# Performance work log

Hardware: AMD Instinct MI355X
Metric: run time of the kernel (lower is better)

Reference implementation:

```python
import jax, jax.numpy as jnp
import numpy as np

B, S, D, H, R, N, KR = 2, 2048, 1024, 16, 256, 8, 128
DH = D // H
EPS = 1e-5


def setup_inputs() -> dict:
    key = jax.random.key(0)
    ks = jax.random.split(key, 20)
    sm = lambda k, n: jax.nn.softmax(jax.random.normal(k, (B, S, n), jnp.float32), axis=-1)
    return {
        "x": jax.random.normal(ks[0], (B, S, D), jnp.float32),
        "fqk_w_Q": sm(ks[1], N),
        "fqk_w_K": sm(ks[2], N),
        "fv_w": sm(ks[3], N),
        "rqk_w_Q": sm(ks[4], N),
        "rqk_w_K": sm(ks[5], N),
        "rv_w": sm(ks[6], N),
        "feature_know_w": sm(ks[7], N),
        "restore_know_w": sm(ks[8], N),
        "f_qk": jax.random.normal(ks[9], (N, D, R), jnp.float32) * 0.02,
        "f_v": jax.random.normal(ks[10], (N, D, R), jnp.float32) * 0.02,
        "r_qk": jax.random.normal(ks[11], (N, R, D), jnp.float32) * 0.02,
        "r_v": jax.random.normal(ks[12], (N, R, D), jnp.float32) * 0.02,
        "f_know": jax.random.normal(ks[13], (N, D, KR), jnp.float32) * 0.02,
        "r_know": jax.random.normal(ks[14], (N, KR, D), jnp.float32) * 0.02,
        "W_O": jax.random.normal(ks[15], (D, D), jnp.float32) * 0.02,
        "ln1_g": jnp.ones((D,), jnp.float32),
        "ln1_b": jnp.zeros((D,), jnp.float32),
        "ln2_g": jnp.ones((D,), jnp.float32),
        "ln2_b": jnp.zeros((D,), jnp.float32),
    }


def _layernorm(x, g, b):
    m = jnp.mean(x, axis=-1, keepdims=True)
    v = jnp.mean(jnp.square(x - m), axis=-1, keepdims=True)
    return (x - m) * jax.lax.rsqrt(v + EPS) * g + b


def _feature(x, neurons, w):
    # fused form of einsum('bsd,ndr->bsnr') + einsum('bsnr,bsn->bsr')
    return jnp.einsum('bsd,bsn,ndr->bsr', x, w, neurons)


def _restore(h, neurons, w):
    # fused form of einsum('bsr,nrd->bsnd') + einsum('bsnd,bsn->bsd')
    return jnp.einsum('bsr,bsn,nrd->bsd', h, w, neurons)


def _causal_sdpa(q, k, v):
    # q,k,v: [B,H,S,DH]
    scores = jnp.einsum('bhqd,bhkd->bhqk', q, k) / jnp.sqrt(jnp.float32(DH))
    mask = jnp.tril(jnp.ones((S, S), bool))
    scores = jnp.where(mask, scores, jnp.finfo(scores.dtype).min)
    p = jax.nn.softmax(scores, axis=-1)
    return jnp.einsum('bhqk,bhkd->bhqd', p, v)


def _block(x, fqk_w_Q, fqk_w_K, fv_w, rqk_w_Q, rqk_w_K, rv_w,
           feature_know_w, restore_know_w, f_qk, f_v, r_qk, r_v,
           f_know, r_know, W_O, ln1_g, ln1_b, ln2_g, ln2_b):
    nx = _layernorm(x, ln1_g, ln1_b)
    h_q = _feature(nx, f_qk, fqk_w_Q)
    h_k = _feature(nx, f_qk, fqk_w_K)
    h_v = _feature(nx, f_v, fv_w)
    Q = _restore(h_q, r_qk, rqk_w_Q)
    K = _restore(h_k, r_qk, rqk_w_K)
    V = _restore(h_v, r_v, rv_w)
    to_heads = lambda t: t.reshape(B, S, H, DH).transpose(0, 2, 1, 3)
    attn = _causal_sdpa(to_heads(Q), to_heads(K), to_heads(V))
    attn = attn.transpose(0, 2, 1, 3).reshape(B, S, D)
    attn_out = attn @ W_O.T  # nn.Linear(d_model,d_model,bias=False)
    x = x + attn_out
    nx2 = _layernorm(x, ln2_g, ln2_b)
    h = _feature(nx2, f_know, feature_know_w)
    know_out = _restore(h, r_know, restore_know_w)
    return x + know_out


def reference(x, fqk_w_Q, fqk_w_K, fv_w, rqk_w_Q, rqk_w_K, rv_w,
              feature_know_w, restore_know_w, f_qk, f_v, r_qk, r_v,
              f_know, r_know, W_O, ln1_g, ln1_b, ln2_g, ln2_b):
    return _block(x, fqk_w_Q, fqk_w_K, fv_w, rqk_w_Q, rqk_w_K, rv_w,
                  feature_know_w, restore_know_w, f_qk, f_v, r_qk, r_v,
                  f_know, r_know, W_O, ln1_g, ln1_b, ln2_g, ln2_b)
```

## Files before the change

### kernel.cpp

```cpp
#include <hip/hip_runtime.h>
#include <hip/hip_bf16.h>


typedef __bf16 bf16_t;
typedef __bf16 bf16x8 __attribute__((ext_vector_type(8)));
typedef float f32x4 __attribute__((ext_vector_type(4)));

#define B_DIM 2
#define S_LEN 2048
#define D_DIM 1024
#define H_NUM 16
#define DH 64
#define N_NEU 8
#define R_DIM 256
#define KR_DIM 128
#define ROWS (B_DIM * S_LEN)

static __device__ __forceinline__ void gl_lds16(const void* g, void* l)
{
    __builtin_amdgcn_global_load_lds(
        (__attribute__((address_space(1))) void*)(g),
        (__attribute__((address_space(3))) void*)(l), 16, 0, 0);
}

__global__ __launch_bounds__(256)
void tcast_kernel(const float* __restrict__ in, bf16_t* __restrict__ out, int I, int J)
{
    __shared__ float t[32][33];
    const int bJ = blockIdx.x * 32, bI = blockIdx.y * 32;
    const size_t boff = (size_t)blockIdx.z * I * J;
    const int tx = threadIdx.x, ty = threadIdx.y;
#pragma unroll
    for (int i = 0; i < 4; i++)
        t[ty * 4 + i][tx] = in[boff + (size_t)(bI + ty * 4 + i) * J + bJ + tx];
    __syncthreads();
#pragma unroll
    for (int i = 0; i < 4; i++)
        out[boff + (size_t)(bJ + ty * 4 + i) * I + bI + tx] = (bf16_t)t[tx][ty * 4 + i];
}

__global__ __launch_bounds__(256)
void tbf_kernel(const bf16_t* __restrict__ in, bf16_t* __restrict__ out, int I, int J)
{
    __shared__ bf16_t t[32][33];
    const int bJ = blockIdx.x * 32, bI = blockIdx.y * 32;
    const size_t boff = (size_t)blockIdx.z * I * J;
    const int tx = threadIdx.x, ty = threadIdx.y;
#pragma unroll
    for (int i = 0; i < 4; i++)
        t[ty * 4 + i][tx] = in[boff + (size_t)(bI + ty * 4 + i) * J + bJ + tx];
    __syncthreads();
#pragma unroll
    for (int i = 0; i < 4; i++)
        out[boff + (size_t)(bJ + ty * 4 + i) * I + bI + tx] = t[tx][ty * 4 + i];
}

__global__ __launch_bounds__(256)
void cast_kernel(const float* __restrict__ in, bf16_t* __restrict__ out, int n4)
{
    int i = blockIdx.x * 256 + threadIdx.x;
    if (i < n4) {
        float4 v = ((const float4*)in)[i];
        bf16_t* op = out + (size_t)i * 4;
        op[0] = (bf16_t)v.x; op[1] = (bf16_t)v.y; op[2] = (bf16_t)v.z; op[3] = (bf16_t)v.w;
    }
}

__global__ __launch_bounds__(256)
void ln_kernel(const float* __restrict__ x, const float* __restrict__ g,
               const float* __restrict__ beta, bf16_t* __restrict__ out)
{
    __shared__ float red[4];
    const int row = blockIdx.x;
    const int tid = threadIdx.x;
    float4 v = *(const float4*)&x[(size_t)row * D_DIM + tid * 4];

    float s = v.x + v.y + v.z + v.w;
#pragma unroll
    for (int o = 32; o; o >>= 1) s += __shfl_down(s, o);
    if ((tid & 63) == 0) red[tid >> 6] = s;
    __syncthreads();
    float mean = (red[0] + red[1] + red[2] + red[3]) * (1.f / D_DIM);
    __syncthreads();

    float dx = v.x - mean, dy = v.y - mean, dz = v.z - mean, dw = v.w - mean;
    float q = dx * dx + dy * dy + dz * dz + dw * dw;
#pragma unroll
    for (int o = 32; o; o >>= 1) q += __shfl_down(q, o);
    if ((tid & 63) == 0) red[tid >> 6] = q;
    __syncthreads();
    float var = (red[0] + red[1] + red[2] + red[3]) * (1.f / D_DIM);
    float rstd = rsqrtf(var + 1e-5f);

    float4 gv = *(const float4*)&g[tid * 4];
    float4 bv = *(const float4*)&beta[tid * 4];
    bf16_t* op = out + (size_t)row * D_DIM + tid * 4;
    op[0] = (bf16_t)(dx * rstd * gv.x + bv.x);
    op[1] = (bf16_t)(dy * rstd * gv.y + bv.y);
    op[2] = (bf16_t)(dz * rstd * gv.z + bv.z);
    op[3] = (bf16_t)(dw * rstd * gv.w + bv.w);
}

__global__ __launch_bounds__(256)
void ln2x_kernel(const float* __restrict__ x, const float* __restrict__ P0,
                 const float* __restrict__ P1, const float* __restrict__ g,
                 const float* __restrict__ beta, float* __restrict__ outf,
                 bf16_t* __restrict__ outn)
{
    __shared__ float red[4];
    const int row = blockIdx.x;
    const int tid = threadIdx.x;
    const size_t base = (size_t)row * D_DIM + tid * 4;
    float4 v  = *(const float4*)&x[base];
    float4 p0 = *(const float4*)&P0[base];
    float4 p1 = *(const float4*)&P1[base];
    v.x += p0.x + p1.x; v.y += p0.y + p1.y; v.z += p0.z + p1.z; v.w += p0.w + p1.w;
    *(float4*)&outf[base] = v;

    float s = v.x + v.y + v.z + v.w;
#pragma unroll
    for (int o = 32; o; o >>= 1) s += __shfl_down(s, o);
    if ((tid & 63) == 0) red[tid >> 6] = s;
    __syncthreads();
    float mean = (red[0] + red[1] + red[2] + red[3]) * (1.f / D_DIM);
    __syncthreads();

    float dx = v.x - mean, dy = v.y - mean, dz = v.z - mean, dw = v.w - mean;
    float q = dx * dx + dy * dy + dz * dz + dw * dw;
#pragma unroll
    for (int o = 32; o; o >>= 1) q += __shfl_down(q, o);
    if ((tid & 63) == 0) red[tid >> 6] = q;
    __syncthreads();
    float var = (red[0] + red[1] + red[2] + red[3]) * (1.f / D_DIM);
    float rstd = rsqrtf(var + 1e-5f);

    float4 gv = *(const float4*)&g[tid * 4];
    float4 bv = *(const float4*)&beta[tid * 4];
    bf16_t* op = outn + base;
    op[0] = (bf16_t)(dx * rstd * gv.x + bv.x);
    op[1] = (bf16_t)(dy * rstd * gv.y + bv.y);
    op[2] = (bf16_t)(dz * rstd * gv.z + bv.z);
    op[3] = (bf16_t)(dw * rstd * gv.w + bv.w);
}

__global__ __launch_bounds__(256)
void wsf_kernel(const bf16_t* __restrict__ y,
                const float* __restrict__ wfQ, const float* __restrict__ wrQ,
                const float* __restrict__ wfK, const float* __restrict__ wrK,
                const float* __restrict__ wfV, const float* __restrict__ wrV,
                bf16_t* __restrict__ sq, bf16_t* __restrict__ sk, bf16_t* __restrict__ sv)
{
    const int r = threadIdx.x;
    const int row = blockIdx.x;
    const bf16_t* yrow = y + (size_t)row * 4096;
    const float* fQ = wfQ + row * N_NEU;
    const float* fK = wfK + row * N_NEU;
    const float* fV = wfV + row * N_NEU;
    float aQ = 0.f, aK = 0.f, aV = 0.f;
#pragma unroll
    for (int n = 0; n < N_NEU; n++) {
        float yq = (float)yrow[n * R_DIM + r];
        float yv = (float)yrow[2048 + n * R_DIM + r];
        aQ += fQ[n] * yq;
        aK += fK[n] * yq;
        aV += fV[n] * yv;
    }
    const float* rQ = wrQ + row * N_NEU;
    const float* rK = wrK + row * N_NEU;
    const float* rV = wrV + row * N_NEU;
    const size_t rb = (size_t)row * 2048;
#pragma unroll
    for (int n = 0; n < N_NEU; n++) {
        sq[rb + n * R_DIM + r] = (bf16_t)(rQ[n] * aQ);
        sk[rb + n * R_DIM + r] = (bf16_t)(rK[n] * aK);
        sv[rb + n * R_DIM + r] = (bf16_t)(rV[n] * aV);
    }
}

__global__ __launch_bounds__(256)
void ws2_kernel(const float* __restrict__ P0, const float* __restrict__ P1,
                const float* __restrict__ wf, const float* __restrict__ wr,
                bf16_t* __restrict__ sout)
{
    const int lr = threadIdx.x >> 7;
    const int r  = threadIdx.x & 127;
    const int row = blockIdx.x * 2 + lr;
    const size_t rb = (size_t)row * (N_NEU * KR_DIM);
    const float* wfp = wf + row * N_NEU;
    const float* wrp = wr + row * N_NEU;
    float acc = 0.f;
#pragma unroll
    for (int n = 0; n < N_NEU; n++) {
        size_t i = rb + n * KR_DIM + r;
        acc += wfp[n] * (P0[i] + P1[i]);
    }
    bf16_t* srow = sout + rb;
#pragma unroll
    for (int n = 0; n < N_NEU; n++) srow[n * KR_DIM + r] = (bf16_t)(wrp[n] * acc);
}

template<int EPI>
__global__ __launch_bounds__(256)
void gemm_kernel(const bf16_t* __restrict__ A, const bf16_t* __restrict__ Bt,
                 const bf16_t* __restrict__ Bt2, int splitMy,
                 void* Cout, const float* resid, int M, int N, int K)
{
    __shared__ bf16_t As[2][128][32];
    __shared__ bf16_t Bs[2][128][32];
    const int tid = threadIdx.x;
    const int l = tid & 63, w = tid >> 6;
    const int wr = w >> 1, wc = w & 1;

    const int nbxy = gridDim.x * gridDim.y;
    int bid = blockIdx.y * gridDim.x + blockIdx.x;
    if ((nbxy & 7) == 0) bid = (bid & 7) * (nbxy >> 3) + (bid >> 3);
    const int bx = bid % gridDim.x, by = bid / gridDim.x;

    const int m0 = by * 128, n0 = bx * 128;
    const bf16_t* Bsel = (by < splitMy) ? Bt : Bt2;

    int kbeg = 0, kend = K;
    if constexpr (EPI == 2) { const int half = K >> 1; kbeg = blockIdx.z * half; kend = kbeg + half; }

    const int srow = l >> 2;
    const int scol = (l & 3) * 8;
    const bf16_t* Ag0 = A    + (size_t)(m0 + w * 32 + srow) * K + scol;
    const bf16_t* Ag1 = Ag0 + (size_t)16 * K;
    const bf16_t* Bg0 = Bsel + (size_t)(n0 + w * 32 + srow) * K + scol;
    const bf16_t* Bg1 = Bg0 + (size_t)16 * K;

    auto stage = [&](int buf, int k0) {
        char* Asb = (char*)&As[buf][0][0] + w * 2048;
        char* Bsb = (char*)&Bs[buf][0][0] + w * 2048;
        gl_lds16(Ag0 + k0, Asb);
        gl_lds16(Ag1 + k0, Asb + 1024);
        gl_lds16(Bg0 + k0, Bsb);
        gl_lds16(Bg1 + k0, Bsb + 1024);
    };

    f32x4 acc[4][4];
    const f32x4 zero = {0.f, 0.f, 0.f, 0.f};
#pragma unroll
    for (int i = 0; i < 4; i++)
#pragma unroll
        for (int j = 0; j < 4; j++) acc[i][j] = zero;

    const int fr = l & 15;
    const int fk = (l >> 4) * 8;

    stage(0, kbeg);
    __syncthreads();

    int cur = 0;
    for (int k0 = kbeg; k0 < kend; k0 += 32) {
        if (k0 + 32 < kend) stage(cur ^ 1, k0 + 32);

        bf16x8 af[4], bv[4];
#pragma unroll
        for (int i = 0; i < 4; i++) af[i] = *(const bf16x8*)&As[cur][wr * 64 + i * 16 + fr][fk];
#pragma unroll
        for (int i = 0; i < 4; i++) bv[i] = *(const bf16x8*)&Bs[cur][wc * 64 + i * 16 + fr][fk];
        __builtin_amdgcn_s_setprio(1);
#pragma unroll
        for (int mi = 0; mi < 4; mi++)
#pragma unroll
            for (int ni = 0; ni < 4; ni++)
                acc[mi][ni] = __builtin_amdgcn_mfma_f32_16x16x32_bf16(af[mi], bv[ni], acc[mi][ni], 0, 0, 0);
        __builtin_amdgcn_s_setprio(0);
        __syncthreads();
        cur ^= 1;
    }

    const int orow = (l >> 4) * 4;
    const int ocol = l & 15;
#pragma unroll
    for (int mi = 0; mi < 4; mi++)
#pragma unroll
        for (int ni = 0; ni < 4; ni++)
#pragma unroll
            for (int j = 0; j < 4; j++) {
                int row = m0 + wr * 64 + mi * 16 + orow + j;
                int col = n0 + wc * 64 + ni * 16 + ocol;
                size_t idx = (size_t)row * N + col;
                if constexpr (EPI == 0) {
                    ((bf16_t*)Cout)[idx] = (bf16_t)acc[mi][ni][j];
                } else if constexpr (EPI == 1) {
                    ((float*)Cout)[idx] = acc[mi][ni][j] + resid[idx];
                } else {
                    ((float*)Cout)[(size_t)blockIdx.z * M * N + idx] = acc[mi][ni][j];
                }
            }
}

__global__ __launch_bounds__(256)
void fa_kernel(const bf16_t* __restrict__ Q, const bf16_t* __restrict__ K,
               const bf16_t* __restrict__ Vt, bf16_t* __restrict__ O)
{
    __shared__ bf16_t Ks[64][72];
    __shared__ bf16_t Vs[64][72];
    __shared__ bf16_t Ps[4][16][72];

    const int tid = threadIdx.x;
    const int l = tid & 63, w = tid >> 6;

    const int bid = blockIdx.x;
    const int xcd  = bid & 7;
    const int slot = bid >> 3;
    const int head = slot & 3;
    const int j5   = slot >> 2;
    const int t5   = j5 & 7, u5 = j5 >> 3;
    const int qb   = 8 * u5 + ((u5 & 1) ? (7 - t5) : t5);
    const int bh   = xcd * 4 + head;
    const int b = bh >> 4, h = bh & 15;
    const int q0 = qb * 64;

    const bf16_t* Qp = Q + (size_t)b * S_LEN * D_DIM + h * DH;
    const bf16_t* Kp = K + (size_t)b * S_LEN * D_DIM + h * DH;
    const bf16_t* Vp = Vt + (size_t)b * D_DIM * S_LEN + (size_t)h * DH * S_LEN;

    const int fr = l & 15, fg = l >> 4, fk = fg * 8;

    bf16x8 qf[2];
#pragma unroll
    for (int ks = 0; ks < 2; ks++)
        qf[ks] = *(const bf16x8*)(Qp + (size_t)(q0 + w * 16 + fr) * D_DIM + ks * 32 + fk);

    bf16x8 ones8;
#pragma unroll
    for (int i = 0; i < 8; i++) ones8[i] = (bf16_t)1.f;

    const f32x4 zero = {0.f, 0.f, 0.f, 0.f};
    f32x4 o[4];
    f32x4 la = zero;
    float m_r[4];
#pragma unroll
    for (int j = 0; j < 4; j++) { o[j] = zero; m_r[j] = -1e30f; }

    const int srow = tid >> 2;
    const int scol = (tid & 3) * 16;
    const bf16_t* Kst = Kp + (size_t)srow * D_DIM + scol;
    const bf16_t* Vst = Vp + (size_t)srow * S_LEN + scol;

    const int nt = q0 / 64 + 1;
    const float C_LOG2 = 0.125f * 1.44269504f;

    uint4 kva = *(const uint4*)(Kst);
    uint4 kvb = *(const uint4*)(Kst + 8);
    uint4 vva = *(const uint4*)(Vst);
    uint4 vvb = *(const uint4*)(Vst + 8);

    for (int t = 0; t < nt; t++) {
        const int k0 = t * 64;
        __syncthreads();
        *(uint4*)&Ks[srow][scol]     = kva;
        *(uint4*)&Ks[srow][scol + 8] = kvb;
        *(uint4*)&Vs[srow][scol]     = vva;
        *(uint4*)&Vs[srow][scol + 8] = vvb;
        __syncthreads();

        if (t + 1 < nt) {
            const int kn = k0 + 64;
            kva = *(const uint4*)(Kst + (size_t)kn * D_DIM);
            kvb = *(const uint4*)(Kst + (size_t)kn * D_DIM + 8);
            vva = *(const uint4*)(Vst + kn);
            vvb = *(const uint4*)(Vst + kn + 8);
        }

        f32x4 sc[4];
#pragma unroll
        for (int ni = 0; ni < 4; ni++) sc[ni] = zero;
        __builtin_amdgcn_s_setprio(1);
#pragma unroll
        for (int ks = 0; ks < 2; ks++) {
#pragma unroll
            for (int ni = 0; ni < 4; ni++) {
                bf16x8 kf = *(const bf16x8*)&Ks[ni * 16 + fr][ks * 32 + fk];
                sc[ni] = __builtin_amdgcn_mfma_f32_16x16x32_bf16(qf[ks], kf, sc[ni], 0, 0, 0);
            }
        }
        __builtin_amdgcn_s_setprio(0);

        float p[4][4];
#pragma unroll
        for (int ni = 0; ni < 4; ni++) {
            const int key = k0 + ni * 16 + fr;
#pragma unroll
            for (int j = 0; j < 4; j++) {
                const int qg = q0 + w * 16 + fg * 4 + j;
                p[ni][j] = (key <= qg) ? sc[ni][j] * C_LOG2 : -1e30f;
            }
        }

#pragma unroll
        for (int j = 0; j < 4; j++) {
            float rmax = fmaxf(fmaxf(p[0][j], p[1][j]), fmaxf(p[2][j], p[3][j]));
#pragma unroll
            for (int d = 1; d < 16; d <<= 1) rmax = fmaxf(rmax, __shfl_xor(rmax, d));
            if (rmax > m_r[j] + 8.f) {
                float scale = exp2f(m_r[j] - rmax);
                la[j] *= scale;
#pragma unroll
                for (int nc = 0; nc < 4; nc++) o[nc][j] *= scale;
                m_r[j] = rmax;
            }
#pragma unroll
            for (int ni = 0; ni < 4; ni++)
                p[ni][j] = exp2f(p[ni][j] - m_r[j]);
        }

#pragma unroll
        for (int ni = 0; ni < 4; ni++)
#pragma unroll
            for (int j = 0; j < 4; j++)
                Ps[w][fg * 4 + j][ni * 16 + fr] = (bf16_t)p[ni][j];

        __builtin_amdgcn_s_setprio(1);
#pragma unroll
        for (int ks = 0; ks < 2; ks++) {
            bf16x8 pa = *(const bf16x8*)&Ps[w][fr][ks * 32 + fk];
            la = __builtin_amdgcn_mfma_f32_16x16x32_bf16(pa, ones8, la, 0, 0, 0);
#pragma unroll
            for (int nc = 0; nc < 4; nc++) {
                bf16x8 vf = *(const bf16x8*)&Vs[nc * 16 + fr][ks * 32 + fk];
                o[nc] = __builtin_amdgcn_mfma_f32_16x16x32_bf16(pa, vf, o[nc], 0, 0, 0);
            }
        }
        __builtin_amdgcn_s_setprio(0);
    }

#pragma unroll
    for (int j = 0; j < 4; j++) {
        const float inv = 1.f / la[j];
        const int q = q0 + w * 16 + fg * 4 + j;
        bf16_t* op = O + (size_t)(b * S_LEN + q) * D_DIM + h * DH;
#pragma unroll
        for (int nc = 0; nc < 4; nc++)
            op[nc * 16 + fr] = (bf16_t)(o[nc][j] * inv);
    }
}

extern "C" void kernel_launch(void* const* d_in, const int* in_sizes, int n_in,
                              void* d_out, int out_size, void* d_ws, size_t ws_size,
                              hipStream_t stream)
{
    const float* x      = (const float*)d_in[0];
    const float* fqk_wQ = (const float*)d_in[1];
    const float* fqk_wK = (const float*)d_in[2];
    const float* fv_w   = (const float*)d_in[3];
    const float* rqk_wQ = (const float*)d_in[4];
    const float* rqk_wK = (const float*)d_in[5];
    const float* rv_w   = (const float*)d_in[6];
    const float* fkn_w  = (const float*)d_in[7];
    const float* rkn_w  = (const float*)d_in[8];
    const float* f_qk   = (const float*)d_in[9];
    const float* f_v    = (const float*)d_in[10];
    const float* r_qk   = (const float*)d_in[11];
    const float* r_v    = (const float*)d_in[12];
    const float* f_know = (const float*)d_in[13];
    const float* r_know = (const float*)d_in[14];
    const float* W_O    = (const float*)d_in[15];
    const float* ln1g   = (const float*)d_in[16];
    const float* ln1b   = (const float*)d_in[17];
    const float* ln2g   = (const float*)d_in[18];
    const float* ln2b   = (const float*)d_in[19];
    float* out_f = (float*)d_out;
    (void)ws_size; (void)in_sizes; (void)n_in; (void)out_size;

    char* ws = (char*)d_ws;
    const size_t MB = 1024 * 1024;
    bf16_t* rqkT   = (bf16_t*)(ws + 0 * MB);
    bf16_t* rvT    = (bf16_t*)(ws + 4 * MB);
    bf16_t* rknT   = (bf16_t*)(ws + 8 * MB);
    bf16_t* woB    = (bf16_t*)(ws + 10 * MB);
    bf16_t* fknT   = (bf16_t*)(ws + 12 * MB);
    bf16_t* buf_nx = (bf16_t*)(ws + 14 * MB);
    bf16_t* buf_y  = (bf16_t*)(ws + 22 * MB);
    char*   buf_s  = ws + 54 * MB;
    bf16_t* fqkT   = (bf16_t*)(buf_s);
    bf16_t* fvT    = (bf16_t*)(buf_s + 4 * MB);
    bf16_t* s_q    = (bf16_t*)(buf_s);
    bf16_t* s_k    = (bf16_t*)(buf_s) + (size_t)4096 * 2048;
    bf16_t* s_v    = (bf16_t*)(buf_s) + (size_t)8192 * 2048;
    bf16_t* attn   = (bf16_t*)(buf_s);
    float*  P0     = (float*)(buf_s + 16 * MB);
    float*  P0k    = (float*)(buf_s);
    float*  P1k    = (float*)(buf_s + 16 * MB);
    bf16_t* sk2    = (bf16_t*)(buf_s + 32 * MB);
    bf16_t* Qb     = buf_y;
    bf16_t* Kb     = buf_y + (size_t)4096 * 1024;
    bf16_t* Vb     = buf_y + (size_t)8192 * 1024;
    bf16_t* Vt     = buf_nx;

    const dim3 blk256(256), blkT(32, 8);

    tcast_kernel<<<dim3(R_DIM / 32, D_DIM / 32, N_NEU), blkT, 0, stream>>>(f_qk, fqkT, D_DIM, R_DIM);
    tcast_kernel<<<dim3(R_DIM / 32, D_DIM / 32, N_NEU), blkT, 0, stream>>>(f_v, fvT, D_DIM, R_DIM);
    tcast_kernel<<<dim3(KR_DIM / 32, D_DIM / 32, N_NEU), blkT, 0, stream>>>(f_know, fknT, D_DIM, KR_DIM);
    tcast_kernel<<<dim3(D_DIM / 32, 2048 / 32, 1), blkT, 0, stream>>>(r_qk, rqkT, 2048, D_DIM);
    tcast_kernel<<<dim3(D_DIM / 32, 2048 / 32, 1), blkT, 0, stream>>>(r_v, rvT, 2048, D_DIM);
    tcast_kernel<<<dim3(D_DIM / 32, 1024 / 32, 1), blkT, 0, stream>>>(r_know, rknT, 1024, D_DIM);
    cast_kernel<<<dim3(1024 * 1024 / 4 / 256), blk256, 0, stream>>>(W_O, woB, 1024 * 1024 / 4);

    ln_kernel<<<dim3(ROWS), blk256, 0, stream>>>(x, ln1g, ln1b, buf_nx);

    gemm_kernel<0><<<dim3(32, 32), blk256, 0, stream>>>(buf_nx, fqkT, fqkT, 1 << 30, buf_y, nullptr, 4096, 4096, 1024);

    wsf_kernel<<<dim3(ROWS), blk256, 0, stream>>>(buf_y, fqk_wQ, rqk_wQ, fqk_wK, rqk_wK, fv_w, rv_w, s_q, s_k, s_v);

    gemm_kernel<0><<<dim3(8, 96), blk256, 0, stream>>>((bf16_t*)buf_s, rqkT, rvT, 64, buf_y, nullptr, 12288, 1024, 2048);

    tbf_kernel<<<dim3(D_DIM / 32, S_LEN / 32, B_DIM), blkT, 0, stream>>>(Vb, Vt, S_LEN, D_DIM);

    fa_kernel<<<dim3(1024), blk256, 0, stream>>>(Qb, Kb, Vt, attn);

    gemm_kernel<2><<<dim3(8, 32, 2), blk256, 0, stream>>>(attn, woB, woB, 1 << 30, P0, nullptr, 4096, 1024, 1024);

    ln2x_kernel<<<dim3(ROWS), blk256, 0, stream>>>(x, P0, P0 + (size_t)4096 * 1024, ln2g, ln2b, out_f, buf_nx);

    gemm_kernel<2><<<dim3(8, 32, 2), blk256, 0, stream>>>(buf_nx, fknT, fknT, 1 << 30, P0k, nullptr, 4096, 1024, 1024);

    ws2_kernel<<<dim3(ROWS / 2), blk256, 0, stream>>>(P0k, P1k, fkn_w, rkn_w, sk2);

    gemm_kernel<1><<<dim3(8, 32), blk256, 0, stream>>>(sk2, rknT, rknT, 1 << 30, d_out, out_f, 4096, 1024, 1024);
}
```

Measured before the change: 330.4 us.

## Triple-buffer GEMM LDS staging and pair causal q-blocks in flash attention

The GEMM kernel moves from double to triple buffering of its async global-to-LDS loads. It waits with explicit vmcnt counts and uses a single barrier per k-step instead of two syncs, so loads stay in flight across the MFMA work. The attention kernel now gives each block two complementary query tiles (31-j and j), which balances causal work across half as many blocks, and it skips the mask computation on off-diagonal tiles. The cost is more LDS per GEMM block, which may reduce occupancy, and a hand-counted waitcnt that depends on how many loads each stage issues.

Result: faster. 317.9 us (-3.8%).

```diff
diff --git a/kernel.cpp b/kernel.cpp
--- a/kernel.cpp
+++ b/kernel.cpp
@@ -205,8 +205,8 @@
                  const bf16_t* __restrict__ Bt2, int splitMy,
                  void* Cout, const float* resid, int M, int N, int K)
 {
-    __shared__ bf16_t As[2][128][32];
-    __shared__ bf16_t Bs[2][128][32];
+    __shared__ bf16_t As[3][128][32];
+    __shared__ bf16_t Bs[3][128][32];
     const int tid = threadIdx.x;
     const int l = tid & 63, w = tid >> 6;
     const int wr = w >> 1, wc = w & 1;
@@ -249,17 +249,27 @@
     const int fk = (l >> 4) * 8;
 
     stage(0, kbeg);
-    __syncthreads();
-
-    int cur = 0;
-    for (int k0 = kbeg; k0 < kend; k0 += 32) {
-        if (k0 + 32 < kend) stage(cur ^ 1, k0 + 32);
-
+    stage(1, kbeg + 32);
+
+    const int nK = (kend - kbeg) >> 5;
+    for (int it = 0; it < nK; ++it) {
+        if (it + 1 < nK) {
+            asm volatile("s_waitcnt vmcnt(4)" ::: "memory");
+        } else {
+            asm volatile("s_waitcnt vmcnt(0)" ::: "memory");
+        }
+        __builtin_amdgcn_s_barrier();
+        __builtin_amdgcn_sched_barrier(0);
+
+        const int cur = it % 3;
         bf16x8 af[4], bv[4];
 #pragma unroll
         for (int i = 0; i < 4; i++) af[i] = *(const bf16x8*)&As[cur][wr * 64 + i * 16 + fr][fk];
 #pragma unroll
         for (int i = 0; i < 4; i++) bv[i] = *(const bf16x8*)&Bs[cur][wc * 64 + i * 16 + fr][fk];
+
+        if (it + 2 < nK) stage((it + 2) % 3, kbeg + (it + 2) * 32);
+
         __builtin_amdgcn_s_setprio(1);
 #pragma unroll
         for (int mi = 0; mi < 4; mi++)
@@ -267,8 +277,6 @@
             for (int ni = 0; ni < 4; ni++)
                 acc[mi][ni] = __builtin_amdgcn_mfma_f32_16x16x32_bf16(af[mi], bv[ni], acc[mi][ni], 0, 0, 0);
         __builtin_amdgcn_s_setprio(0);
-        __syncthreads();
-        cur ^= 1;
     }
 
     const int orow = (l >> 4) * 4;
@@ -303,139 +311,148 @@
     const int tid = threadIdx.x;
     const int l = tid & 63, w = tid >> 6;
 
-    const int bid = blockIdx.x;
+    const int bid  = blockIdx.x;
     const int xcd  = bid & 7;
     const int slot = bid >> 3;
     const int head = slot & 3;
-    const int j5   = slot >> 2;
-    const int t5   = j5 & 7, u5 = j5 >> 3;
-    const int qb   = 8 * u5 + ((u5 & 1) ? (7 - t5) : t5);
+    const int jq   = slot >> 2;
     const int bh   = xcd * 4 + head;
     const int b = bh >> 4, h = bh & 15;
-    const int q0 = qb * 64;
 
     const bf16_t* Qp = Q + (size_t)b * S_LEN * D_DIM + h * DH;
     const bf16_t* Kp = K + (size_t)b * S_LEN * D_DIM + h * DH;
     const bf16_t* Vp = Vt + (size_t)b * D_DIM * S_LEN + (size_t)h * DH * S_LEN;
 
     const int fr = l & 15, fg = l >> 4, fk = fg * 8;
-
-    bf16x8 qf[2];
-#pragma unroll
-    for (int ks = 0; ks < 2; ks++)
-        qf[ks] = *(const bf16x8*)(Qp + (size_t)(q0 + w * 16 + fr) * D_DIM + ks * 32 + fk);
-
-    bf16x8 ones8;
-#pragma unroll
-    for (int i = 0; i < 8; i++) ones8[i] = (bf16_t)1.f;
-
-    const f32x4 zero = {0.f, 0.f, 0.f, 0.f};
-    f32x4 o[4];
-    f32x4 la = zero;
-    float m_r[4];
-#pragma unroll
-    for (int j = 0; j < 4; j++) { o[j] = zero; m_r[j] = -1e30f; }
-
     const int srow = tid >> 2;
     const int scol = (tid & 3) * 16;
     const bf16_t* Kst = Kp + (size_t)srow * D_DIM + scol;
     const bf16_t* Vst = Vp + (size_t)srow * S_LEN + scol;
 
-    const int nt = q0 / 64 + 1;
+    bf16x8 ones8;
+#pragma unroll
+    for (int i = 0; i < 8; i++) ones8[i] = (bf16_t)1.f;
+
+    const f32x4 zero = {0.f, 0.f, 0.f, 0.f};
     const float C_LOG2 = 0.125f * 1.44269504f;
 
-    uint4 kva = *(const uint4*)(Kst);
-    uint4 kvb = *(const uint4*)(Kst + 8);
-    uint4 vva = *(const uint4*)(Vst);
-    uint4 vvb = *(const uint4*)(Vst + 8);
-
-    for (int t = 0; t < nt; t++) {
-        const int k0 = t * 64;
-        __syncthreads();
-        *(uint4*)&Ks[srow][scol]     = kva;
-        *(uint4*)&Ks[srow][scol + 8] = kvb;
-        *(uint4*)&Vs[srow][scol]     = vva;
-        *(uint4*)&Vs[srow][scol + 8] = vvb;
-        __syncthreads();
-
-        if (t + 1 < nt) {
-            const int kn = k0 + 64;
-            kva = *(const uint4*)(Kst + (size_t)kn * D_DIM);
-            kvb = *(const uint4*)(Kst + (size_t)kn * D_DIM + 8);
-            vva = *(const uint4*)(Vst + kn);
-            vvb = *(const uint4*)(Vst + kn + 8);
+    for (int pass = 0; pass < 2; ++pass) {
+        const int qb = pass ? jq : (31 - jq);
+        const int q0 = qb * 64;
+        const int nt = qb + 1;
+
+        bf16x8 qf[2];
+#pragma unroll
+        for (int ks = 0; ks < 2; ks++)
+            qf[ks] = *(const bf16x8*)(Qp + (size_t)(q0 + w * 16 + fr) * D_DIM + ks * 32 + fk);
+
+        f32x4 o[4];
+        f32x4 la = zero;
+        float m_r[4];
+#pragma unroll
+        for (int j = 0; j < 4; j++) { o[j] = zero; m_r[j] = -1e30f; }
+
+        uint4 kva = *(const uint4*)(Kst);
+        uint4 kvb = *(const uint4*)(Kst + 8);
+        uint4 vva = *(const uint4*)(Vst);
+        uint4 vvb = *(const uint4*)(Vst + 8);
+
+        for (int t = 0; t < nt; t++) {
+            const int k0 = t * 64;
+            __syncthreads();
+            *(uint4*)&Ks[srow][scol]     = kva;
+            *(uint4*)&Ks[srow][scol + 8] = kvb;
+            *(uint4*)&Vs[srow][scol]     = vva;
+            *(uint4*)&Vs[srow][scol + 8] = vvb;
+            __syncthreads();
+
+            if (t + 1 < nt) {
+                const int kn = k0 + 64;
+                kva = *(const uint4*)(Kst + (size_t)kn * D_DIM);
+                kvb = *(const uint4*)(Kst + (size_t)kn * D_DIM + 8);
+                vva = *(const uint4*)(Vst + kn);
+                vvb = *(const uint4*)(Vst + kn + 8);
+            }
+
+            f32x4 sc[4];
+#pragma unroll
+            for (int ni = 0; ni < 4; ni++) sc[ni] = zero;
+            __builtin_amdgcn_s_setprio(1);
+#pragma unroll
+            for (int ks = 0; ks < 2; ks++) {
+#pragma unroll
+                for (int ni = 0; ni < 4; ni++) {
+                    bf16x8 kf = *(const bf16x8*)&Ks[ni * 16 + fr][ks * 32 + fk];
+                    sc[ni] = __builtin_amdgcn_mfma_f32_16x16x32_bf16(qf[ks], kf, sc[ni], 0, 0, 0);
+                }
+            }
+            __builtin_amdgcn_s_setprio(0);
+
+            float p[4][4];
+            if (t == qb) {
+#pragma unroll
+                for (int ni = 0; ni < 4; ni++) {
+                    const int key = k0 + ni * 16 + fr;
+#pragma unroll
+                    for (int j = 0; j < 4; j++) {
+                        const int qg = q0 + w * 16 + fg * 4 + j;
+                        p[ni][j] = (key <= qg) ? sc[ni][j] * C_LOG2 : -1e30f;
+                    }
+                }
+            } else {
+#pragma unroll
+                for (int ni = 0; ni < 4; ni++)
+#pragma unroll
+                    for (int j = 0; j < 4; j++)
+                        p[ni][j] = sc[ni][j] * C_LOG2;
+            }
+
+#pragma unroll
+            for (int j = 0; j < 4; j++) {
+                float rmax = fmaxf(fmaxf(p[0][j], p[1][j]), fmaxf(p[2][j], p[3][j]));
+#pragma unroll
+                for (int d = 1; d < 16; d <<= 1) rmax = fmaxf(rmax, __shfl_xor(rmax, d));
+                if (rmax > m_r[j] + 8.f) {
+                    float scale = exp2f(m_r[j] - rmax);
+                    la[j] *= scale;
+#pragma unroll
+                    for (int nc = 0; nc < 4; nc++) o[nc][j] *= scale;
+                    m_r[j] = rmax;
+                }
+#pragma unroll
+                for (int ni = 0; ni < 4; ni++)
+                    p[ni][j] = exp2f(p[ni][j] - m_r[j]);
+            }
+
+#pragma unroll
+            for (int ni = 0; ni < 4; ni++)
+#pragma unroll
+                for (int j = 0; j < 4; j++)
+                    Ps[w][fg * 4 + j][ni * 16 + fr] = (bf16_t)p[ni][j];
+
+            __builtin_amdgcn_s_setprio(1);
+#pragma unroll
+            for (int ks = 0; ks < 2; ks++) {
+                bf16x8 pa = *(const bf16x8*)&Ps[w][fr][ks * 32 + fk];
+                la = __builtin_amdgcn_mfma_f32_16x16x32_bf16(pa, ones8, la, 0, 0, 0);
+#pragma unroll
+                for (int nc = 0; nc < 4; nc++) {
+                    bf16x8 vf = *(const bf16x8*)&Vs[nc * 16 + fr][fk + ks * 32];
+                    o[nc] = __builtin_amdgcn_mfma_f32_16x16x32_bf16(pa, vf, o[nc], 0, 0, 0);
+                }
+            }
+            __builtin_amdgcn_s_setprio(0);
         }
 
-        f32x4 sc[4];
-#pragma unroll
-        for (int ni = 0; ni < 4; ni++) sc[ni] = zero;
-        __builtin_amdgcn_s_setprio(1);
-#pragma unroll
-        for (int ks = 0; ks < 2; ks++) {
-#pragma unroll
-            for (int ni = 0; ni < 4; ni++) {
-                bf16x8 kf = *(const bf16x8*)&Ks[ni * 16 + fr][ks * 32 + fk];
-                sc[ni] = __builtin_amdgcn_mfma_f32_16x16x32_bf16(qf[ks], kf, sc[ni], 0, 0, 0);
-            }
+#pragma unroll
+        for (int j = 0; j < 4; j++) {
+            const float inv = 1.f / la[j];
+            const int q = q0 + w * 16 + fg * 4 + j;
+            bf16_t* op = O + (size_t)(b * S_LEN + q) * D_DIM + h * DH;
+#pragma unroll
+            for (int nc = 0; nc < 4; nc++)
+                op[nc * 16 + fr] = (bf16_t)(o[nc][j] * inv);
         }
-        __builtin_amdgcn_s_setprio(0);
-
-        float p[4][4];
-#pragma unroll
-        for (int ni = 0; ni < 4; ni++) {
-            const int key = k0 + ni * 16 + fr;
-#pragma unroll
-            for (int j = 0; j < 4; j++) {
-                const int qg = q0 + w * 16 + fg * 4 + j;
-                p[ni][j] = (key <= qg) ? sc[ni][j] * C_LOG2 : -1e30f;
-            }
-        }
-
-#pragma unroll
-        for (int j = 0; j < 4; j++) {
-            float rmax = fmaxf(fmaxf(p[0][j], p[1][j]), fmaxf(p[2][j], p[3][j]));
-#pragma unroll
-            for (int d = 1; d < 16; d <<= 1) rmax = fmaxf(rmax, __shfl_xor(rmax, d));
-            if (rmax > m_r[j] + 8.f) {
-                float scale = exp2f(m_r[j] - rmax);
-                la[j] *= scale;
-#pragma unroll
-                for (int nc = 0; nc < 4; nc++) o[nc][j] *= scale;
-                m_r[j] = rmax;
-            }
-#pragma unroll
-            for (int ni = 0; ni < 4; ni++)
-                p[ni][j] = exp2f(p[ni][j] - m_r[j]);
-        }
-
-#pragma unroll
-        for (int ni = 0; ni < 4; ni++)
-#pragma unroll
-            for (int j = 0; j < 4; j++)
-                Ps[w][fg * 4 + j][ni * 16 + fr] = (bf16_t)p[ni][j];
-
-        __builtin_amdgcn_s_setprio(1);
-#pragma unroll
-        for (int ks = 0; ks < 2; ks++) {
-            bf16x8 pa = *(const bf16x8*)&Ps[w][fr][ks * 32 + fk];
-            la = __builtin_amdgcn_mfma_f32_16x16x32_bf16(pa, ones8, la, 0, 0, 0);
-#pragma unroll
-            for (int nc = 0; nc < 4; nc++) {
-                bf16x8 vf = *(const bf16x8*)&Vs[nc * 16 + fr][ks * 32 + fk];
-                o[nc] = __builtin_amdgcn_mfma_f32_16x16x32_bf16(pa, vf, o[nc], 0, 0, 0);
-            }
-        }
-        __builtin_amdgcn_s_setprio(0);
-    }
-
-#pragma unroll
-    for (int j = 0; j < 4; j++) {
-        const float inv = 1.f / la[j];
-        const int q = q0 + w * 16 + fg * 4 + j;
-        bf16_t* op = O + (size_t)(b * S_LEN + q) * D_DIM + h * DH;
-#pragma unroll
-        for (int nc = 0; nc < 4; nc++)
-            op[nc * 16 + fr] = (bf16_t)(o[nc][j] * inv);
     }
 }
 
@@ -511,7 +528,7 @@
 
     tbf_kernel<<<dim3(D_DIM / 32, S_LEN / 32, B_DIM), blkT, 0, stream>>>(Vb, Vt, S_LEN, D_DIM);
 
-    fa_kernel<<<dim3(1024), blk256, 0, stream>>>(Qb, Kb, Vt, attn);
+    fa_kernel<<<dim3(512), blk256, 0, stream>>>(Qb, Kb, Vt, attn);
 
     gemm_kernel<2><<<dim3(8, 32, 2), blk256, 0, stream>>>(attn, woB, woB, 1 << 30, P0, nullptr, 4096, 1024, 1024);
 
```
